# Performance work log

Hardware: AMD Instinct MI355X
Metric: run time of the kernel (lower is better)

Reference implementation:

```python
import jax, jax.numpy as jnp
import numpy as np

N_EVENTS = 16
N_SAMPLES = 2 ** 15          # 32768
STEP = 256                   # window_size // 2
LONG_WINDOW = 4096
LONG_COEFFS = LONG_WINDOW // 2 + 1   # 2049
LONG_STEP = LONG_WINDOW // 2         # 2048
LONG_FRAMES = N_SAMPLES // LONG_STEP # 16
N_FRAMES = N_SAMPLES // STEP         # 128
B = 8                                 # audio batch
BE = B * N_EVENTS                     # event batch = 128


def setup_inputs() -> dict:
    key = jax.random.key(0)
    k1, k2, k3, k4 = jax.random.split(key, 4)
    env = jax.random.uniform(k1, (BE, LONG_WINDOW, LONG_FRAMES), jnp.float32)
    tf = jax.random.normal(k2, (BE, LONG_COEFFS * 2, LONG_FRAMES), jnp.float32)
    noise = jax.random.uniform(k3, (BE, LONG_WINDOW, LONG_FRAMES), jnp.float32)
    indices = jax.random.randint(k4, (B, N_EVENTS), 0, N_FRAMES, dtype=jnp.int32)
    return {"env": env, "tf": tf, "noise": noise, "indices": indices}


def _event_render(env, tf, noise):
    # env, noise: (BE, LONG_WINDOW, LONG_FRAMES); tf: (BE, 2*LONG_COEFFS, LONG_FRAMES)
    batch = env.shape[0]
    energy = env * (noise * 2.0 - 1.0)  # uniform_(-1, 1) noise scaled by amp

    # magnitude = norm over interleaved (real, imag) pairs, per torch view semantics
    pairs = tf.reshape(batch, LONG_COEFFS, 2, LONG_FRAMES)
    mag = jnp.sqrt(jnp.sum(pairs * pairs, axis=2))  # (batch, C, F)
    mx = jnp.max(mag.reshape(batch, -1), axis=-1, keepdims=True)
    mag = (mag.reshape(batch, -1) / (mx + 1e-8)).reshape(batch, LONG_COEFFS, LONG_FRAMES)
    imag = tf[:, LONG_COEFFS:, :]
    phase = jnp.arctan2(imag, mag) * np.pi  # torch.angle(complex(mag, imag)) * pi
    tfc = mag * jnp.exp(1j * phase)         # complex transfer fn (batch, C, F)

    # sequential per-frame recurrence: state feeds through rfft/irfft filtering
    e_t = jnp.transpose(energy, (2, 0, 1))  # (F, batch, W)
    t_t = jnp.transpose(tfc, (2, 0, 1))     # (F, batch, C)

    def step(prev, inp):
        e, t = inp
        local = prev + e
        spec = jnp.fft.rfft(local, axis=-1, norm='ortho') * t
        frame = jnp.fft.irfft(spec, n=LONG_WINDOW, axis=-1, norm='ortho')
        return frame, frame

    init = jnp.zeros((batch, LONG_WINDOW), energy.dtype)
    _, frames = jax.lax.scan(step, init, (e_t, t_t))   # (F, batch, W)
    frames = jnp.transpose(frames, (1, 0, 2))          # (batch, F, W)

    # overlap-add with hop = LONG_STEP = W/2: split frames into halves and add
    halves = frames.reshape(batch, LONG_FRAMES, 2, LONG_STEP)
    out = jnp.zeros((batch, LONG_FRAMES + 1, LONG_STEP), frames.dtype)
    out = out.at[:, :LONG_FRAMES].add(halves[:, :, 0])
    out = out.at[:, 1:].add(halves[:, :, 1])
    return out.reshape(batch, -1)[:, :N_SAMPLES]       # (BE, N_SAMPLES)


def _segment_render(atoms, indices):
    # atoms: (BE, N_SAMPLES) -> (B, N_EVENTS, N_SAMPLES); scatter-add at time offsets
    x = atoms.reshape(B, N_EVENTS, N_SAMPLES)
    times = indices * STEP                                      # (B, E)
    pos = times[:, :, None] + jnp.arange(N_SAMPLES)[None, None, :]  # (B, E, S)
    out = jnp.zeros((B, 2 * N_SAMPLES), x.dtype)
    bidx = jnp.arange(B)[:, None, None]
    out = out.at[bidx, pos].add(x)
    return out[:, None, :N_SAMPLES]                             # (B, 1, N_SAMPLES)


def reference(env, tf, noise, indices):
    atoms = _event_render(env, tf, noise)
    return _segment_render(atoms, indices)
```

## Files before the change

### kernel.cpp

```cpp
#include <hip/hip_runtime.h>
#include <hip/hip_fp16.h>
#include <math.h>

#define TWO_PI 6.283185307179586f

#define OFF_F    0ull
#define OFF_E    4194304ull
#define OFF_MAXP 8390656ull
#define OFF_Z    8391680ull

__device__ __forceinline__ int swz(int n) { return n ^ ((n >> 5) & 31); }

__device__ __forceinline__ int permf(int k) {
    return ((k & 1) << 10) | (((k >> 1) & 3) << 8) | (((k >> 3) & 3) << 6)
         | (((k >> 5) & 3) << 4) | (((k >> 7) & 3) << 2) | ((k >> 9) & 3);
}

__device__ __forceinline__ void r4f_core(float* cr, float* ci, int p0, int p1, int p2, int p3,
                                         float c1, float s1, float c2, float s2, float c3, float s3) {
    float ar = cr[p0], ai = ci[p0];
    float br = cr[p1], bi = ci[p1];
    float crr = cr[p2], cri = ci[p2];
    float drr = cr[p3], dri = ci[p3];
    float u0r = ar + crr, u0i = ai + cri;
    float u1r = ar - crr, u1i = ai - cri;
    float u2r = br + drr, u2i = bi + dri;
    float u3r = br - drr, u3i = bi - dri;
    cr[p0] = u0r + u2r; ci[p0] = u0i + u2i;
    float z1r = u1r + u3i, z1i = u1i - u3r;
    cr[p1] = z1r * c1 + z1i * s1; ci[p1] = z1i * c1 - z1r * s1;
    float z2r = u0r - u2r, z2i = u0i - u2i;
    cr[p2] = z2r * c2 + z2i * s2; ci[p2] = z2i * c2 - z2r * s2;
    float z3r = u1r - u3i, z3i = u1i + u3r;
    cr[p3] = z3r * c3 + z3i * s3; ci[p3] = z3i * c3 - z3r * s3;
}

__device__ __forceinline__ void r4i_core(float* cr, float* ci, int p0, int p1, int p2, int p3,
                                         float c1, float s1, float c2, float s2, float c3, float s3) {
    float z0r = cr[p0], z0i = ci[p0];
    float z1r = cr[p1], z1i = ci[p1];
    float z2r = cr[p2], z2i = ci[p2];
    float z3r = cr[p3], z3i = ci[p3];
    float t1r = z1r * c1 - z1i * s1, t1i = z1i * c1 + z1r * s1;
    float t2r = z2r * c2 - z2i * s2, t2i = z2i * c2 + z2r * s2;
    float t3r = z3r * c3 - z3i * s3, t3i = z3i * c3 + z3r * s3;
    float u0r = z0r + t2r, u0i = z0i + t2i;
    float u1r = z0r - t2r, u1i = z0i - t2i;
    float u2r = t1r + t3r, u2i = t1i + t3i;
    float u3r = t1r - t3r, u3i = t1i - t3i;
    cr[p0] = u0r + u2r; ci[p0] = u0i + u2i;
    cr[p1] = u1r - u3i; ci[p1] = u1i + u3r;
    cr[p2] = u0r - u2r; ci[p2] = u0i - u2i;
    cr[p3] = u1r + u3i; ci[p3] = u1i - u3r;
}

#define STAGE4X(CORE, JEXPR, H, ANGEXPR)                                       \
    {                                                                          \
        _Pragma("unroll")                                                      \
        for (int half_ = 0; half_ < 2; ++half_) {                              \
            int b_ = tid + half_ * 1024;                                       \
            int i_ = b_ & 511;                                                 \
            float* cr_ = B + (b_ >> 9) * 4096;                                 \
            float* ci_ = cr_ + 2048;                                           \
            int j_ = (JEXPR);                                                  \
            int p0 = swz(j_), p1 = swz(j_ + (H)), p2 = swz(j_ + 2 * (H)),      \
                p3 = swz(j_ + 3 * (H));                                        \
            float s1, c1; __sincosf((ANGEXPR), &s1, &c1);                      \
            float c2 = c1 * c1 - s1 * s1, s2 = 2.f * c1 * s1;                  \
            float c3 = c1 * c2 - s1 * s2, s3 = s1 * c2 + c1 * s2;              \
            CORE(cr_, ci_, p0, p1, p2, p3, c1, s1, c2, s2, c3, s3);            \
        }                                                                      \
    }                                                                          \
    __syncthreads();

__global__ __launch_bounds__(1024, 8) void k_fwd(const float* __restrict__ env,
                                                 const float* __restrict__ noise,
                                                 const float* __restrict__ tf,
                                                 float* __restrict__ ws) {
    __shared__ float B[16384];
    int tid = threadIdx.x;
    int id = blockIdx.x;
    int xcd = id & 7, slot = id >> 3;
    int be = xcd * 16 + (slot >> 2);
    int fg = slot & 3;
    const float4* env4 = (const float4*)env;
    const float4* noi4 = (const float4*)noise;
    size_t base = (size_t)be * 16384 + fg;
#pragma unroll
    for (int it = 0; it < 4; ++it) {
        int n = it * 1024 + tid;
        float4 e = env4[base + (size_t)n * 4];
        float4 z = noi4[base + (size_t)n * 4];
        float v0 = e.x * (z.x * 2.0f - 1.0f);
        float v1 = e.y * (z.y * 2.0f - 1.0f);
        float v2 = e.z * (z.z * 2.0f - 1.0f);
        float v3 = e.w * (z.w * 2.0f - 1.0f);
        int m = swz(n >> 1) + (n & 1) * 2048;
        B[m] = v0; B[4096 + m] = v1; B[8192 + m] = v2; B[12288 + m] = v3;
    }
    __syncthreads();
    {
        int i = tid;
        int sj = swz(i), sjb = swz(i + 1024);
        float s, c; __sincosf((float)i * (TWO_PI / 2048.0f), &s, &c);
#pragma unroll
        for (int j4 = 0; j4 < 4; ++j4) {
            float* cr = B + j4 * 4096;
            float* ci = cr + 2048;
            float ar = cr[sj], ai = ci[sj], br = cr[sjb], bi = ci[sjb];
            float dr = ar - br, di = ai - bi;
            cr[sj] = ar + br; ci[sj] = ai + bi;
            cr[sjb] = dr * c + di * s; ci[sjb] = di * c - dr * s;
        }
    }
    __syncthreads();
    STAGE4X(r4f_core, (i_ >> 8) * 1024 + (i_ & 255), 256, (float)(i_ & 255) * (TWO_PI / 1024.0f));
    STAGE4X(r4f_core, (i_ >> 6) * 256 + (i_ & 63), 64, (float)(i_ & 63) * (TWO_PI / 256.0f));
    STAGE4X(r4f_core, (i_ & 31) * 64 + (i_ >> 5), 16, (float)(i_ >> 5) * (TWO_PI / 64.0f));
    STAGE4X(r4f_core, (i_ & 127) * 16 + (i_ >> 7), 4, (float)(i_ >> 7) * (TWO_PI / 16.0f));
    STAGE4X(r4f_core, i_ * 4, 1, 0.0f);
    __half2* Ebase = (__half2*)(ws + OFF_E) + (size_t)(be * 16 + fg * 4) * 2049;
    for (int k = tid; k <= 1024; k += 1024) {
        int pk = swz(permf(k));
        int pm = swz(permf((2048 - k) & 2047));
        float s4, c4; __sincosf((float)k * (TWO_PI / 4096.0f), &s4, &c4);
#pragma unroll
        for (int j4 = 0; j4 < 4; ++j4) {
            float* cr = B + j4 * 4096;
            float* ci = cr + 2048;
            float zkr = cr[pk], zki = ci[pk], zmr = cr[pm], zmi = ci[pm];
            float xer = 0.5f * (zkr + zmr), xei = 0.5f * (zki - zmi);
            float xor_ = 0.5f * (zki + zmi), xoi = 0.5f * (zmr - zkr);
            float wr = xor_ * c4 + xoi * s4;
            float wi = xoi * c4 - xor_ * s4;
            __half2* Eg = Ebase + (size_t)j4 * 2049;
            Eg[k] = __floats2half2_rn(xer + wr, xei + wi);
            Eg[2048 - k] = __floats2half2_rn(xer - wr, wi - xei);
        }
    }
    __syncthreads();
    const float4* ab4 = (const float4*)(tf + (size_t)be * 65568);
    int b0 = fg * 513;
    int nb = (fg == 3) ? 510 : 513;
    float mx = 0.f;
    for (int u = tid; u < nb * 4; u += 1024) {
        int g = u >> 2, e = u & 3;
        int bin = b0 + g;
        float4 A = ab4[bin * 8 + e];
        float4 Bv = ab4[bin * 8 + e + 4];
        mx = fmaxf(mx, fmaxf(fmaxf(A.x * A.x + Bv.x * Bv.x, A.y * A.y + Bv.y * Bv.y),
                             fmaxf(A.z * A.z + Bv.z * Bv.z, A.w * A.w + Bv.w * Bv.w)));
    }
    B[tid] = mx;
    __syncthreads();
    for (int s = 512; s > 0; s >>= 1) {
        if (tid < s) B[tid] = fmaxf(B[tid], B[tid + s]);
        __syncthreads();
    }
    if (tid == 0) ws[OFF_MAXP + be * 4 + fg] = B[0];
}

__global__ __launch_bounds__(256) void k_recur(const float* __restrict__ tf,
                                               float* __restrict__ ws) {
    __shared__ float sm2lo[256 * 17], simlo[256 * 17];
    __shared__ float sm2hi[256 * 17], simhi[256 * 17];
    int tid = threadIdx.x;
    int be = blockIdx.y;
    int k0 = blockIdx.x << 8;
    int hi0 = 1793 - k0;
    const float* tfb = tf + (size_t)be * 65568;
    const float4* ab4 = (const float4*)tfb;
    const float4* im4 = (const float4*)(tfb + 32784);

    for (int u = tid; u < 2048; u += 256) {
        int half = u >> 10, v = u & 1023;
        int g = v >> 2, e = v & 3;
        int bin = half ? (hi0 + g) : (k0 + g);
        float4 A = ab4[bin * 8 + e];
        float4 Bv = ab4[bin * 8 + e + 4];
        float4 I = im4[bin * 4 + e];
        int o = g * 17 + e * 4;
        float* sm = half ? sm2hi : sm2lo;
        float* si = half ? simhi : simlo;
        sm[o + 0] = A.x * A.x + Bv.x * Bv.x;
        sm[o + 1] = A.y * A.y + Bv.y * Bv.y;
        sm[o + 2] = A.z * A.z + Bv.z * Bv.z;
        sm[o + 3] = A.w * A.w + Bv.w * Bv.w;
        si[o + 0] = I.x; si[o + 1] = I.y; si[o + 2] = I.z; si[o + 3] = I.w;
    }
    __syncthreads();

    int k = k0 + tid;
    int m = 2048 - k;
    int rhi = 255 - tid;
    const float* mp = ws + OFF_MAXP + be * 4;
    float m2x = fmaxf(fmaxf(mp[0], mp[1]), fmaxf(mp[2], mp[3]));
    float rden = 1.0f / (sqrtf(m2x) + 1e-8f);
    const __half2* Eb = (const __half2*)(ws + OFF_E) + (size_t)be * 16 * 2049;
    __half2* Zb = (__half2*)(ws + OFF_Z) + (size_t)be * 16 * 2048;
    float2 evlo[16], evhi[16];
#pragma unroll
    for (int f = 0; f < 16; ++f) {
        evlo[f] = __half22float2(Eb[(size_t)f * 2049 + k]);
        evhi[f] = __half22float2(Eb[(size_t)f * 2049 + m]);
    }
    float ym = (k == 0) ? 0.0f : 1.0f;
    float s4, c4; __sincosf((float)k * (TWO_PI / 4096.0f), &s4, &c4);
    const float SCL = 1.0f / 2048.0f;
    float srl = 0.f, sil = 0.f, srh = 0.f, sih = 0.f;
#pragma unroll
    for (int f = 0; f < 16; ++f) {
        float mh = sqrtf(sm2lo[tid * 17 + f]) * rden;
        float ph = atan2f(simlo[tid * 17 + f], mh) * 3.14159265358979f;
        float sp, cp; __sincosf(ph, &sp, &cp);
        float Tr = mh * cp, Ti = mh * sp;
        sil *= ym;
        srl += evlo[f].x; sil += evlo[f].y;
        float nr = srl * Tr - sil * Ti;
        sil = srl * Ti + sil * Tr; srl = nr;
        float mh2 = sqrtf(sm2hi[rhi * 17 + f]) * rden;
        float ph2 = atan2f(simhi[rhi * 17 + f], mh2) * 3.14159265358979f;
        float sp2, cp2; __sincosf(ph2, &sp2, &cp2);
        float Tr2 = mh2 * cp2, Ti2 = mh2 * sp2;
        sih *= ym;
        srh += evhi[f].x; sih += evhi[f].y;
        float nr2 = srh * Tr2 - sih * Ti2;
        sih = srh * Ti2 + sih * Tr2; srh = nr2;
        __half2* Zf = Zb + (size_t)f * 2048;
        if (k == 0) {
            float y0 = srl * SCL, yn = srh * SCL;
            Zf[0] = __floats2half2_rn(0.5f * (y0 + yn), 0.5f * (y0 - yn));
        } else {
            float ykr = srl * SCL, yki = sil * SCL;
            float ymr = srh * SCL, ymi = sih * SCL;
            float er = 0.5f * (ykr + ymr), ei = 0.5f * (yki - ymi);
            float dr = ykr - ymr, di = yki + ymi;
            float orr = 0.5f * (dr * c4 - di * s4);
            float oi = 0.5f * (dr * s4 + di * c4);
            Zf[k] = __floats2half2_rn(er - oi, ei + orr);
            Zf[m] = __floats2half2_rn(er + oi, orr - ei);
        }
    }
    if (k0 == 0 && tid == 0) {
        float sr = 0.f, si = 0.f;
#pragma unroll
        for (int f = 0; f < 16; ++f) {
            float a = tfb[1024 * 32 + f];
            float b = tfb[1024 * 32 + 16 + f];
            float im = tfb[32784 + 1024 * 16 + f];
            float mh = sqrtf(a * a + b * b) * rden;
            float ph = atan2f(im, mh) * 3.14159265358979f;
            float sp, cp; __sincosf(ph, &sp, &cp);
            float Tr = mh * cp, Ti = mh * sp;
            float2 e = __half22float2(Eb[(size_t)f * 2049 + 1024]);
            sr += e.x; si += e.y;
            float nr = sr * Tr - si * Ti;
            si = sr * Ti + si * Tr; sr = nr;
            Zb[(size_t)f * 2048 + 1024] = __floats2half2_rn(sr * SCL, -si * SCL);
        }
    }
}

__global__ __launch_bounds__(1024, 8) void k_fft_inv(float* __restrict__ ws) {
    __shared__ float B[16384];
    int tid = threadIdx.x;
    int be = blockIdx.x >> 2, fg = blockIdx.x & 3;
    const __half2* Zbase = (const __half2*)(ws + OFF_Z) + (size_t)(be * 16 + fg * 4) * 2048;
    {
        int n0 = tid * 2;
        int p0 = swz(permf(n0)), p1 = swz(permf(n0 + 1));
#pragma unroll
        for (int j4 = 0; j4 < 4; ++j4) {
            uint2 raw = ((const uint2*)(Zbase + (size_t)j4 * 2048))[tid];
            float2 v0 = __half22float2(*(const __half2*)&raw.x);
            float2 v1 = __half22float2(*(const __half2*)&raw.y);
            float* cr = B + j4 * 4096;
            float* ci = cr + 2048;
            cr[p0] = v0.x; ci[p0] = v0.y;
            cr[p1] = v1.x; ci[p1] = v1.y;
        }
    }
    __syncthreads();
    STAGE4X(r4i_core, i_ * 4, 1, 0.0f);
    STAGE4X(r4i_core, (i_ & 127) * 16 + (i_ >> 7), 4, (float)(i_ >> 7) * (TWO_PI / 16.0f));
    STAGE4X(r4i_core, (i_ & 31) * 64 + (i_ >> 5), 16, (float)(i_ >> 5) * (TWO_PI / 64.0f));
    STAGE4X(r4i_core, (i_ >> 6) * 256 + (i_ & 63), 64, (float)(i_ & 63) * (TWO_PI / 256.0f));
    STAGE4X(r4i_core, (i_ >> 8) * 1024 + (i_ & 255), 256, (float)(i_ & 255) * (TWO_PI / 1024.0f));
    {
        int i = tid;
        int sj = swz(i), sjb = swz(i + 1024);
        float s, c; __sincosf((float)i * (TWO_PI / 2048.0f), &s, &c);
#pragma unroll
        for (int j4 = 0; j4 < 4; ++j4) {
            float* cr = B + j4 * 4096;
            float* ci = cr + 2048;
            float br = cr[sjb], bi = ci[sjb];
            float tr = br * c - bi * s, ti2 = br * s + bi * c;
            float ar = cr[sj], ai = ci[sj];
            cr[sj] = ar + tr;  ci[sj] = ai + ti2;
            cr[sjb] = ar - tr; ci[sjb] = ai - ti2;
        }
    }
    __syncthreads();
    __half2* Fbase = (__half2*)(ws + OFF_F) + (size_t)(be * 16 + fg * 4) * 2048;
#pragma unroll
    for (int j4 = 0; j4 < 4; ++j4) {
        float* cr = B + j4 * 4096;
        float* ci = cr + 2048;
        __half2* Fg = Fbase + (size_t)j4 * 2048;
#pragma unroll
        for (int it = 0; it < 2; ++it) {
            int m = tid + it * 1024;
            Fg[m] = __floats2half2_rn(cr[swz(m)], ci[swz(m)]);
        }
    }
}

__global__ __launch_bounds__(256) void k_segment(const float* __restrict__ ws,
                                                 const int* __restrict__ indices,
                                                 float* __restrict__ out) {
    __shared__ int ste[16];
    int tid = threadIdx.x;
    int b = blockIdx.y;
    if (tid < 16) ste[tid] = indices[b * 16 + tid] * 256;
    __syncthreads();
    int g = blockIdx.x * 256 + tid;
    int t = g << 2;
    const __half* F = (const __half*)(ws + OFF_F);
    float4 acc = make_float4(0.f, 0.f, 0.f, 0.f);
#pragma unroll
    for (int e = 0; e < 16; ++e) {
        int te = ste[e];
        if (t >= te) {
            int d = t - te;
            int j = d >> 11, r = d & 2047;
            size_t base = (size_t)(b * 16 + e) * 65536;
            uint2 raw = *(const uint2*)(F + base + j * 4096 + r);
            float2 a0 = __half22float2(*(const __half2*)&raw.x);
            float2 a1 = __half22float2(*(const __half2*)&raw.y);
            acc.x += a0.x; acc.y += a0.y; acc.z += a1.x; acc.w += a1.y;
            if (j >= 1) {
                uint2 rw2 = *(const uint2*)(F + base + (j - 1) * 4096 + 2048 + r);
                float2 b0 = __half22float2(*(const __half2*)&rw2.x);
                float2 b1 = __half22float2(*(const __half2*)&rw2.y);
                acc.x += b0.x; acc.y += b0.y; acc.z += b1.x; acc.w += b1.y;
            }
        }
    }
    ((float4*)out)[(size_t)b * 8192 + g] = acc;
}

extern "C" void kernel_launch(void* const* d_in, const int* in_sizes, int n_in,
                              void* d_out, int out_size, void* d_ws, size_t ws_size,
                              hipStream_t stream) {
    const float* env = (const float*)d_in[0];
    const float* tf = (const float*)d_in[1];
    const float* noise = (const float*)d_in[2];
    const int* indices = (const int*)d_in[3];
    float* ws = (float*)d_ws;
    float* out = (float*)d_out;

    k_fwd<<<dim3(512), dim3(1024), 0, stream>>>(env, noise, tf, ws);
    k_recur<<<dim3(4, 128), dim3(256), 0, stream>>>(tf, ws);
    k_fft_inv<<<dim3(512), dim3(1024), 0, stream>>>(ws);
    k_segment<<<dim3(32, 8), dim3(256), 0, stream>>>(ws, indices, out);
}
```

Before: 76.75 us.

## Store inverse FFT in packed half2 shared memory and fuse first/last stages

The inverse FFT kernel now keeps intermediate values in shared memory as packed half2 instead of separate float real/imag arrays. This halves LDS size and traffic and lets the output stage write straight to global without an extra barrier. The forward kernel fuses the input load with the first butterfly stage in registers, removing one shared-memory round trip and a barrier. Rounding every inverse FFT stage to half precision costs accuracy.

```diff
diff --git a/kernel.cpp b/kernel.cpp
--- a/kernel.cpp
+++ b/kernel.cpp
@@ -14,6 +14,15 @@
 __device__ __forceinline__ int permf(int k) {
     return ((k & 1) << 10) | (((k >> 1) & 3) << 8) | (((k >> 3) & 3) << 6)
          | (((k >> 5) & 3) << 4) | (((k >> 7) & 3) << 2) | ((k >> 9) & 3);
+}
+
+__device__ __forceinline__ float2 uph(unsigned u) {
+    __half2 h = *(__half2*)&u;
+    return __half22float2(h);
+}
+__device__ __forceinline__ unsigned pkh(float x, float y) {
+    __half2 h = __floats2half2_rn(x, y);
+    return *(unsigned*)&h;
 }
 
 __device__ __forceinline__ void r4f_core(float* cr, float* ci, int p0, int p1, int p2, int p3,
@@ -35,23 +44,20 @@
     cr[p3] = z3r * c3 + z3i * s3; ci[p3] = z3i * c3 - z3r * s3;
 }
 
-__device__ __forceinline__ void r4i_core(float* cr, float* ci, int p0, int p1, int p2, int p3,
-                                         float c1, float s1, float c2, float s2, float c3, float s3) {
-    float z0r = cr[p0], z0i = ci[p0];
-    float z1r = cr[p1], z1i = ci[p1];
-    float z2r = cr[p2], z2i = ci[p2];
-    float z3r = cr[p3], z3i = ci[p3];
-    float t1r = z1r * c1 - z1i * s1, t1i = z1i * c1 + z1r * s1;
-    float t2r = z2r * c2 - z2i * s2, t2i = z2i * c2 + z2r * s2;
-    float t3r = z3r * c3 - z3i * s3, t3i = z3i * c3 + z3r * s3;
-    float u0r = z0r + t2r, u0i = z0i + t2i;
-    float u1r = z0r - t2r, u1i = z0i - t2i;
+__device__ __forceinline__ void r4i_pk(unsigned* b, int p0, int p1, int p2, int p3,
+                                       float c1, float s1, float c2, float s2, float c3, float s3) {
+    float2 z0 = uph(b[p0]), z1 = uph(b[p1]), z2 = uph(b[p2]), z3 = uph(b[p3]);
+    float t1r = z1.x * c1 - z1.y * s1, t1i = z1.y * c1 + z1.x * s1;
+    float t2r = z2.x * c2 - z2.y * s2, t2i = z2.y * c2 + z2.x * s2;
+    float t3r = z3.x * c3 - z3.y * s3, t3i = z3.y * c3 + z3.x * s3;
+    float u0r = z0.x + t2r, u0i = z0.y + t2i;
+    float u1r = z0.x - t2r, u1i = z0.y - t2i;
     float u2r = t1r + t3r, u2i = t1i + t3i;
     float u3r = t1r - t3r, u3i = t1i - t3i;
-    cr[p0] = u0r + u2r; ci[p0] = u0i + u2i;
-    cr[p1] = u1r - u3i; ci[p1] = u1i + u3r;
-    cr[p2] = u0r - u2r; ci[p2] = u0i - u2i;
-    cr[p3] = u1r + u3i; ci[p3] = u1i - u3r;
+    b[p0] = pkh(u0r + u2r, u0i + u2i);
+    b[p1] = pkh(u1r - u3i, u1i + u3r);
+    b[p2] = pkh(u0r - u2r, u0i - u2i);
+    b[p3] = pkh(u1r + u3i, u1i - u3r);
 }
 
 #define STAGE4X(CORE, JEXPR, H, ANGEXPR)                                       \
@@ -73,6 +79,24 @@
     }                                                                          \
     __syncthreads();
 
+#define STAGE4P(JEXPR, H, ANGEXPR)                                             \
+    {                                                                          \
+        _Pragma("unroll")                                                      \
+        for (int half_ = 0; half_ < 2; ++half_) {                              \
+            int b_ = tid + half_ * 1024;                                       \
+            int i_ = b_ & 511;                                                 \
+            unsigned* bb_ = B2 + (b_ >> 9) * 2048;                             \
+            int j_ = (JEXPR);                                                  \
+            int p0 = swz(j_), p1 = swz(j_ + (H)), p2 = swz(j_ + 2 * (H)),      \
+                p3 = swz(j_ + 3 * (H));                                        \
+            float s1, c1; __sincosf((ANGEXPR), &s1, &c1);                      \
+            float c2 = c1 * c1 - s1 * s1, s2 = 2.f * c1 * s1;                  \
+            float c3 = c1 * c2 - s1 * s2, s3 = s1 * c2 + c1 * s2;              \
+            r4i_pk(bb_, p0, p1, p2, p3, c1, s1, c2, s2, c3, s3);               \
+        }                                                                      \
+    }                                                                          \
+    __syncthreads();
+
 __global__ __launch_bounds__(1024, 8) void k_fwd(const float* __restrict__ env,
                                                  const float* __restrict__ noise,
                                                  const float* __restrict__ tf,
@@ -86,31 +110,41 @@
     const float4* env4 = (const float4*)env;
     const float4* noi4 = (const float4*)noise;
     size_t base = (size_t)be * 16384 + fg;
-#pragma unroll
-    for (int it = 0; it < 4; ++it) {
-        int n = it * 1024 + tid;
-        float4 e = env4[base + (size_t)n * 4];
-        float4 z = noi4[base + (size_t)n * 4];
-        float v0 = e.x * (z.x * 2.0f - 1.0f);
-        float v1 = e.y * (z.y * 2.0f - 1.0f);
-        float v2 = e.z * (z.z * 2.0f - 1.0f);
-        float v3 = e.w * (z.w * 2.0f - 1.0f);
-        int m = swz(n >> 1) + (n & 1) * 2048;
-        B[m] = v0; B[4096 + m] = v1; B[8192 + m] = v2; B[12288 + m] = v3;
-    }
-    __syncthreads();
+
     {
-        int i = tid;
-        int sj = swz(i), sjb = swz(i + 1024);
-        float s, c; __sincosf((float)i * (TWO_PI / 2048.0f), &s, &c);
+        float4 ea0 = env4[base + (size_t)(2 * tid) * 4];
+        float4 ea1 = env4[base + (size_t)(2 * tid + 1) * 4];
+        float4 eb0 = env4[base + (size_t)(2 * tid + 2048) * 4];
+        float4 eb1 = env4[base + (size_t)(2 * tid + 2049) * 4];
+        float4 za0 = noi4[base + (size_t)(2 * tid) * 4];
+        float4 za1 = noi4[base + (size_t)(2 * tid + 1) * 4];
+        float4 zb0 = noi4[base + (size_t)(2 * tid + 2048) * 4];
+        float4 zb1 = noi4[base + (size_t)(2 * tid + 2049) * 4];
+        float4 A0 = make_float4(ea0.x * (za0.x * 2.f - 1.f), ea0.y * (za0.y * 2.f - 1.f),
+                                ea0.z * (za0.z * 2.f - 1.f), ea0.w * (za0.w * 2.f - 1.f));
+        float4 A1 = make_float4(ea1.x * (za1.x * 2.f - 1.f), ea1.y * (za1.y * 2.f - 1.f),
+                                ea1.z * (za1.z * 2.f - 1.f), ea1.w * (za1.w * 2.f - 1.f));
+        float4 B0 = make_float4(eb0.x * (zb0.x * 2.f - 1.f), eb0.y * (zb0.y * 2.f - 1.f),
+                                eb0.z * (zb0.z * 2.f - 1.f), eb0.w * (zb0.w * 2.f - 1.f));
+        float4 B1 = make_float4(eb1.x * (zb1.x * 2.f - 1.f), eb1.y * (zb1.y * 2.f - 1.f),
+                                eb1.z * (zb1.z * 2.f - 1.f), eb1.w * (zb1.w * 2.f - 1.f));
+        const float* A0v = (const float*)&A0;
+        const float* A1v = (const float*)&A1;
+        const float* B0v = (const float*)&B0;
+        const float* B1v = (const float*)&B1;
+        float s, c; __sincosf((float)tid * (TWO_PI / 2048.0f), &s, &c);
+        int pj = swz(tid), pjb = swz(tid + 1024);
 #pragma unroll
         for (int j4 = 0; j4 < 4; ++j4) {
+            float xr = A0v[j4], xi = A1v[j4];
+            float yr = B0v[j4], yi = B1v[j4];
+            float ar = xr + yr, ai = xi + yi;
+            float dr = xr - yr, di = xi - yi;
             float* cr = B + j4 * 4096;
             float* ci = cr + 2048;
-            float ar = cr[sj], ai = ci[sj], br = cr[sjb], bi = ci[sjb];
-            float dr = ar - br, di = ai - bi;
-            cr[sj] = ar + br; ci[sj] = ai + bi;
-            cr[sjb] = dr * c + di * s; ci[sjb] = di * c - dr * s;
+            cr[pj] = ar; ci[pj] = ai;
+            cr[pjb] = dr * c + di * s;
+            ci[pjb] = di * c - dr * s;
         }
     }
     __syncthreads();
@@ -262,7 +296,7 @@
 }
 
 __global__ __launch_bounds__(1024, 8) void k_fft_inv(float* __restrict__ ws) {
-    __shared__ float B[16384];
+    __shared__ unsigned B2[8192];
     int tid = threadIdx.x;
     int be = blockIdx.x >> 2, fg = blockIdx.x & 3;
     const __half2* Zbase = (const __half2*)(ws + OFF_Z) + (size_t)(be * 16 + fg * 4) * 2048;
@@ -272,46 +306,30 @@
 #pragma unroll
         for (int j4 = 0; j4 < 4; ++j4) {
             uint2 raw = ((const uint2*)(Zbase + (size_t)j4 * 2048))[tid];
-            float2 v0 = __half22float2(*(const __half2*)&raw.x);
-            float2 v1 = __half22float2(*(const __half2*)&raw.y);
-            float* cr = B + j4 * 4096;
-            float* ci = cr + 2048;
-            cr[p0] = v0.x; ci[p0] = v0.y;
-            cr[p1] = v1.x; ci[p1] = v1.y;
-        }
-    }
-    __syncthreads();
-    STAGE4X(r4i_core, i_ * 4, 1, 0.0f);
-    STAGE4X(r4i_core, (i_ & 127) * 16 + (i_ >> 7), 4, (float)(i_ >> 7) * (TWO_PI / 16.0f));
-    STAGE4X(r4i_core, (i_ & 31) * 64 + (i_ >> 5), 16, (float)(i_ >> 5) * (TWO_PI / 64.0f));
-    STAGE4X(r4i_core, (i_ >> 6) * 256 + (i_ & 63), 64, (float)(i_ & 63) * (TWO_PI / 256.0f));
-    STAGE4X(r4i_core, (i_ >> 8) * 1024 + (i_ & 255), 256, (float)(i_ & 255) * (TWO_PI / 1024.0f));
+            unsigned* bb = B2 + j4 * 2048;
+            bb[p0] = raw.x;
+            bb[p1] = raw.y;
+        }
+    }
+    __syncthreads();
+    STAGE4P(i_ * 4, 1, 0.0f);
+    STAGE4P((i_ & 127) * 16 + (i_ >> 7), 4, (float)(i_ >> 7) * (TWO_PI / 16.0f));
+    STAGE4P((i_ & 31) * 64 + (i_ >> 5), 16, (float)(i_ >> 5) * (TWO_PI / 64.0f));
+    STAGE4P((i_ >> 6) * 256 + (i_ & 63), 64, (float)(i_ & 63) * (TWO_PI / 256.0f));
+    STAGE4P((i_ >> 8) * 1024 + (i_ & 255), 256, (float)(i_ & 255) * (TWO_PI / 1024.0f));
     {
-        int i = tid;
-        int sj = swz(i), sjb = swz(i + 1024);
-        float s, c; __sincosf((float)i * (TWO_PI / 2048.0f), &s, &c);
+        int sj = swz(tid), sjb = swz(tid + 1024);
+        float s, c; __sincosf((float)tid * (TWO_PI / 2048.0f), &s, &c);
+        __half2* Fbase = (__half2*)(ws + OFF_F) + (size_t)(be * 16 + fg * 4) * 2048;
 #pragma unroll
         for (int j4 = 0; j4 < 4; ++j4) {
-            float* cr = B + j4 * 4096;
-            float* ci = cr + 2048;
-            float br = cr[sjb], bi = ci[sjb];
-            float tr = br * c - bi * s, ti2 = br * s + bi * c;
-            float ar = cr[sj], ai = ci[sj];
-            cr[sj] = ar + tr;  ci[sj] = ai + ti2;
-            cr[sjb] = ar - tr; ci[sjb] = ai - ti2;
-        }
-    }
-    __syncthreads();
-    __half2* Fbase = (__half2*)(ws + OFF_F) + (size_t)(be * 16 + fg * 4) * 2048;
-#pragma unroll
-    for (int j4 = 0; j4 < 4; ++j4) {
-        float* cr = B + j4 * 4096;
-        float* ci = cr + 2048;
-        __half2* Fg = Fbase + (size_t)j4 * 2048;
-#pragma unroll
-        for (int it = 0; it < 2; ++it) {
-            int m = tid + it * 1024;
-            Fg[m] = __floats2half2_rn(cr[swz(m)], ci[swz(m)]);
+            unsigned* bb = B2 + j4 * 2048;
+            float2 a = uph(bb[sj]);
+            float2 b = uph(bb[sjb]);
+            float tr = b.x * c - b.y * s, ti2 = b.x * s + b.y * c;
+            __half2* Fg = Fbase + (size_t)j4 * 2048;
+            Fg[tid] = __floats2half2_rn(a.x + tr, a.y + ti2);
+            Fg[tid + 1024] = __floats2half2_rn(a.x - tr, a.y - ti2);
         }
     }
 }
```

New measurement: 78.27 us. About the same (+2.0%).
